# Kernel optimization log

Measured on AMD Instinct MI355X. Metric: run time of the kernel, lower is better.

Reference implementation:

```python
import jax, jax.numpy as jnp
import numpy as np

NUM_EMBEDDINGS = 1024
EMBEDDING_DIM = 256
BETA = 0.25


def setup_inputs() -> dict:
    key = jax.random.key(0)
    k1, k2 = jax.random.split(key)
    x = jax.random.normal(k1, (32, 256, 32, 32), dtype=jnp.float32)
    # nn.Embedding weight init: uniform(-1/K, 1/K)
    lim = 1.0 / NUM_EMBEDDINGS
    emb_weight = jax.random.uniform(k2, (NUM_EMBEDDINGS, EMBEDDING_DIM),
                                    dtype=jnp.float32, minval=-lim, maxval=lim)
    return {"x": x, "emb_weight": emb_weight}


def reference(x, emb_weight):
    b, c, h, w = x.shape
    # [b, h, w, c] -> [N, c]
    x_flat = jnp.transpose(x, (0, 2, 3, 1)).reshape(-1, c)
    distances = (jnp.sum(x_flat * x_flat, axis=1, keepdims=True)
                 - 2.0 * jnp.einsum('nc,kc->nk', x_flat, emb_weight)
                 + jnp.sum(emb_weight * emb_weight, axis=1))
    indices = jnp.argmin(distances, axis=1)  # [N]
    quantized = emb_weight[indices].reshape(b, h, w, c).transpose(0, 3, 1, 2)
    sg = jax.lax.stop_gradient
    commitment_loss = jnp.mean((sg(quantized) - x) ** 2)
    embedding_loss = jnp.mean((quantized - sg(x)) ** 2)
    loss = commitment_loss + BETA * embedding_loss
    return quantized, loss, indices.reshape(b, h, w)
```

## Files before the change

kernel.cpp:

```cpp
#include <hip/hip_runtime.h>

#define LOSS_OFF 8388608
#define IDX_OFF  8388609

#define WS_SEE   0
#define WS_SXX   4096
#define WS_KEY   135168
#define WS_CNT   397312
#define WS_LOSS  397320
#define WS_WL    397328
#define WS_EP    528448

#define FLT_BIG  3.402823466e+38f
#define MARGIN   1.0e-4f

typedef __attribute__((ext_vector_type(8))) short  short8v;
typedef __attribute__((ext_vector_type(4))) float  float4v;

#define GLD16(gp, lp) __builtin_amdgcn_global_load_lds( \
    (const __attribute__((address_space(1))) unsigned int*)(gp), \
    (__attribute__((address_space(3))) unsigned int*)(lp), 16, 0, 0)

__device__ __forceinline__ float np_sumsq256(const float* __restrict__ p, int stride) {
    float s[2];
#pragma unroll
    for (int half = 0; half < 2; half++) {
        const float* a = p + half * 128 * stride;
        float r[8];
#pragma unroll
        for (int l = 0; l < 8; l++) {
            float v = a[l * stride];
            float sq = v * v;
            asm volatile("" : "+v"(sq));
            r[l] = sq;
        }
#pragma unroll
        for (int i = 8; i < 128; i += 8) {
#pragma unroll
            for (int l = 0; l < 8; l++) {
                float v = a[(i + l) * stride];
                float sq = v * v;
                asm volatile("" : "+v"(sq));
                r[l] = r[l] + sq;
            }
        }
        s[half] = ((r[0] + r[1]) + (r[2] + r[3])) + ((r[4] + r[5]) + (r[6] + r[7]));
    }
    return s[0] + s[1];
}

__device__ __forceinline__ unsigned int f32_sortable(float m) {
    unsigned int u = __float_as_uint(m);
    return u ^ (((unsigned int)((int)u >> 31)) | 0x80000000u);
}
__device__ __forceinline__ float f32_unsortable(unsigned int s) {
    const unsigned int u = (s >> 31) ? (s ^ 0x80000000u) : ~s;
    return __uint_as_float(u);
}

__device__ __forceinline__ unsigned short f2bf(float f) {
    unsigned int u = __float_as_uint(f);
    return (unsigned short)((u + 0x7fffu + ((u >> 16) & 1u)) >> 16);
}
__device__ __forceinline__ float bf2f(unsigned short h) {
    return __uint_as_float(((unsigned int)h) << 16);
}

__global__ __launch_bounds__(256) void k_prep(const float* __restrict__ emb,
                                              unsigned short* __restrict__ ebP,
                                              float* __restrict__ see,
                                              int* __restrict__ cnt,
                                              double* __restrict__ loss) {
    const int t = threadIdx.x, bb = blockIdx.x;
    if (bb < 256) {
        const int idx = bb * 256 + t;
        const int l  = idx & 63;
        const int ph = (idx >> 6) & 1;
        const int ct = (idx >> 7) & 7;
        const int cc = (idx >> 10) & 7;
        const int cg = (idx >> 13) & 7;
        const int row = cg * 128 + ct * 16 + (l & 15);
        const int col = cc * 32 + (l >> 4) * 8;
        const float* src = emb + (size_t)row * 256 + col;
        uint4 out;
        unsigned short* op = (unsigned short*)&out;
#pragma unroll
        for (int i = 0; i < 8; i++) {
            const float v = src[i];
            const unsigned short h = f2bf(v);
            op[i] = ph ? f2bf(v - bf2f(h)) : h;
        }
        *(uint4*)(ebP + (size_t)idx * 8) = out;
    } else {
        const int k = (bb - 256) * 256 + t;
        see[k] = np_sumsq256(emb + (size_t)k * 256, 1);
        if (k == 0) { *cnt = 0; *loss = 0.0; }
    }
}

__global__ __launch_bounds__(256) void k_et(const float* __restrict__ emb,
                                            float* __restrict__ eT) {
    __shared__ float T[256][17];
    const int t  = threadIdx.x;
    const int k0 = blockIdx.x << 4;
    const int kr = t >> 4, cs = (t & 15) << 4;
#pragma unroll
    for (int j = 0; j < 4; j++) {
        const float4 v = *(const float4*)(emb + (size_t)(k0 + kr) * 256 + cs + j * 4);
        T[cs + j * 4 + 0][kr] = v.x;
        T[cs + j * 4 + 1][kr] = v.y;
        T[cs + j * 4 + 2][kr] = v.z;
        T[cs + j * 4 + 3][kr] = v.w;
    }
    __syncthreads();
    float* dst = eT + (size_t)t * 1024 + k0;
#pragma unroll
    for (int j = 0; j < 4; j++) {
        float4 v;
        v.x = T[t][j * 4 + 0]; v.y = T[t][j * 4 + 1];
        v.z = T[t][j * 4 + 2]; v.w = T[t][j * 4 + 3];
        *(float4*)(dst + j * 4) = v;
    }
}

__global__ __launch_bounds__(256) void k_xpack(const float* __restrict__ x,
                                               unsigned short* __restrict__ axP,
                                               float* __restrict__ sxx) {
    __shared__ float xs[256 * 33];
    const int t = threadIdx.x, rs = blockIdx.x;
    const int row = t & 31, cg = t >> 5;
    const int b = rs >> 5;
    const int hw0 = (rs & 31) << 5;
    const float* xb = x + (size_t)b * 262144 + hw0 + row;
#pragma unroll 4
    for (int cc2 = 0; cc2 < 32; cc2++) {
        const int c = cg * 32 + cc2;
        xs[c * 33 + row] = xb[(size_t)c * 1024];
    }
    __syncthreads();
#pragma unroll
    for (int ii = 0; ii < 4; ii++) {
        const int ci = ii * 256 + t;
        const int l = ci & 63;
        const int rowg = (ci >> 6) & 1;
        const int cc = ci >> 7;
        const int r = rowg * 16 + (l & 15);
        const int c0 = cc * 32 + (l >> 4) * 8;
        uint4 hp, lp;
        unsigned short* hpp = (unsigned short*)&hp;
        unsigned short* lpp = (unsigned short*)&lp;
#pragma unroll
        for (int i = 0; i < 8; i++) {
            const float v = xs[(c0 + i) * 33 + r];
            const unsigned short h = f2bf(v);
            hpp[i] = h;
            lpp[i] = f2bf(v - bf2f(h));
        }
        const size_t base = ((size_t)rs * 8 + cc) * 2 + rowg;
        *(uint4*)(axP + ((base * 2 + 0) * 64 + l) * 8) = hp;
        *(uint4*)(axP + ((base * 2 + 1) * 64 + l) * 8) = lp;
    }
    if (t < 32) sxx[rs * 32 + t] = np_sumsq256(xs + t, 33);
}

__global__ __launch_bounds__(512, 2) void k1_mfma(
        const unsigned short* __restrict__ axP,
        const unsigned short* __restrict__ ebP,
        const float* __restrict__ see_g,
        unsigned long long* __restrict__ key,
        int* __restrict__ cnt, int* __restrict__ wl) {
    __shared__ char smem[8192];
    unsigned long long* lk1 = (unsigned long long*)smem;
    float*              lg2 = (float*)(smem + 4096);
    const int t = threadIdx.x;
    const int codeg = t >> 6, l = t & 63;
    const int lrow = l >> 4, lcol = l & 15;
    const int rb = blockIdx.x;
    const int n0 = rb * 64;
    const char* aBase = (const char*)axP;
    char* aDst = smem + codeg * 1024;

    float4v acc[4][8];
#pragma unroll
    for (int at = 0; at < 4; at++)
#pragma unroll
        for (int ct = 0; ct < 8; ct++) acc[at][ct] = (float4v){0.f, 0.f, 0.f, 0.f};

    for (int cc = 0; cc < 8; cc++) {
        __syncthreads();
        {
            const int sub = codeg >> 2;
            const char* src = aBase + ((size_t)((rb * 2 + sub) * 8 + cc)) * 4096
                              + (size_t)(codeg & 3) * 1024 + (size_t)l * 16;
            GLD16(src, aDst);
        }
        __syncthreads();
        short8v ah[4], al[4];
#pragma unroll
        for (int at = 0; at < 4; at++) {
            const int off = (at >> 1) * 4096 + (at & 1) * 2048;
            ah[at] = *(const short8v*)(smem + off + l * 16);
            al[at] = *(const short8v*)(smem + off + 1024 + l * 16);
        }
#pragma unroll
        for (int ct = 0; ct < 8; ct++) {
            const size_t bb = ((((size_t)codeg * 8 + cc) * 8 + ct) * 2) * 512 + (size_t)l * 8;
            const short8v bh = *(const short8v*)(ebP + bb);
            const short8v bl = *(const short8v*)(ebP + bb + 512);
#pragma unroll
            for (int at = 0; at < 4; at++) {
                acc[at][ct] = __builtin_amdgcn_mfma_f32_16x16x32_bf16(ah[at], bh, acc[at][ct], 0, 0, 0);
                acc[at][ct] = __builtin_amdgcn_mfma_f32_16x16x32_bf16(ah[at], bl, acc[at][ct], 0, 0, 0);
                acc[at][ct] = __builtin_amdgcn_mfma_f32_16x16x32_bf16(al[at], bh, acc[at][ct], 0, 0, 0);
            }
        }
    }
    __syncthreads();

    float sv[8];
#pragma unroll
    for (int ct = 0; ct < 8; ct++) sv[ct] = see_g[codeg * 128 + ct * 16 + lcol];

#pragma unroll
    for (int at = 0; at < 4; at++) {
#pragma unroll
        for (int j = 0; j < 4; j++) {
            unsigned long long K1 = ~0ull; float G1 = FLT_BIG, G2 = FLT_BIG;
#pragma unroll
            for (int ct = 0; ct < 8; ct++) {
                const float g = fmaf(-2.f, acc[at][ct][j], sv[ct]);
                const int k = codeg * 128 + ct * 16 + lcol;
                const unsigned long long pk =
                    ((unsigned long long)f32_sortable(g) << 32) | (unsigned int)k;
                if (pk < K1) { G2 = G1; K1 = pk; G1 = g; }
                else         { G2 = fminf(G2, g); }
            }
#pragma unroll
            for (int m = 1; m < 16; m <<= 1) {
                const unsigned long long oK = __shfl_xor(K1, m, 64);
                const float oG2 = __shfl_xor(G2, m, 64);
                const float oG1 = f32_unsortable((unsigned int)(oK >> 32));
                if (oK < K1) { G2 = fminf(oG2, G1); K1 = oK; G1 = oG1; }
                else         { G2 = fminf(G2, oG1); }
            }
            const int rloc = at * 16 + lrow * 4 + j;
            if (lcol == 0) { lk1[rloc * 8 + codeg] = K1; lg2[rloc * 8 + codeg] = G2; }
        }
    }
    __syncthreads();
    if (t < 64) {
        unsigned long long K1 = ~0ull; float G1 = FLT_BIG, G2 = FLT_BIG;
        for (int cg = 0; cg < 8; cg++) {
            const unsigned long long oK = lk1[t * 8 + cg];
            const float oG2 = lg2[t * 8 + cg];
            const float oG1 = f32_unsortable((unsigned int)(oK >> 32));
            if (oK < K1) { G2 = fminf(oG2, G1); K1 = oK; G1 = oG1; }
            else         { G2 = fminf(G2, oG1); }
        }
        const int n = n0 + t;
        if (G2 - G1 > MARGIN) { key[n] = K1; }
        else { key[n] = ~0ull; wl[atomicAdd(cnt, 1)] = n; }
    }
}

__global__ __launch_bounds__(256) void k2r(const float* __restrict__ x,
                                           const float* __restrict__ eT,
                                           const float* __restrict__ see,
                                           const float* __restrict__ sxx,
                                           unsigned long long* __restrict__ key,
                                           const int* __restrict__ cnt,
                                           const int* __restrict__ wl) {
    __shared__ float xs[8][264];
    const int t = threadIdx.x;
    const int total = *cnt;
    for (int base = blockIdx.x * 8; base < total; base += 128 * 8) {
        int nrow[8]; float sx8[8];
#pragma unroll
        for (int r = 0; r < 8; r++) {
            int idx = base + r; if (idx >= total) idx = total - 1;
            const int n = wl[idx];
            nrow[r] = n; sx8[r] = sxx[n];
        }
        __syncthreads();
#pragma unroll
        for (int r = 0; r < 8; r++) {
            const int n = nrow[r];
            xs[r][t] = x[(size_t)(n >> 10) * 262144 + (size_t)t * 1024 + (n & 1023)];
        }
        __syncthreads();
        float d[8][4];
#pragma unroll
        for (int r = 0; r < 8; r++)
#pragma unroll
            for (int j = 0; j < 4; j++) d[r][j] = 0.f;
#pragma unroll 4
        for (int c = 0; c < 256; c++) {
            float ev[4];
#pragma unroll
            for (int j = 0; j < 4; j++) ev[j] = eT[(size_t)c * 1024 + t + 256 * j];
#pragma unroll
            for (int r = 0; r < 8; r++) {
                const float xv = xs[r][c];
                d[r][0] = fmaf(xv, ev[0], d[r][0]);
                d[r][1] = fmaf(xv, ev[1], d[r][1]);
                d[r][2] = fmaf(xv, ev[2], d[r][2]);
                d[r][3] = fmaf(xv, ev[3], d[r][3]);
            }
        }
#pragma unroll
        for (int r = 0; r < 8; r++) {
            unsigned long long best = ~0ull;
#pragma unroll
            for (int j = 0; j < 4; j++) {
                const float q = fmaf(-2.f, d[r][j], sx8[r]) + see[t + 256 * j];
                const unsigned long long pk =
                    ((unsigned long long)f32_sortable(q) << 32) | (unsigned int)(t + 256 * j);
                best = pk < best ? pk : best;
            }
            atomicMin(&key[nrow[r]], best);
        }
    }
}

__global__ __launch_bounds__(256) void k3_out(const float* __restrict__ x,
                                              const float* __restrict__ emb,
                                              const unsigned long long* __restrict__ key,
                                              float* __restrict__ dout,
                                              double* __restrict__ loss) {
    __shared__ float elds[32][257];
    __shared__ int   idxs[32];
    __shared__ float red[256];
    const int t  = threadIdx.x;
    const int bh = blockIdx.x;
    const int b = bh >> 5, h = bh & 31;
    if (t < 32) idxs[t] = (int)(key[(bh << 5) + t] & 0xffffffffull);
    __syncthreads();
    for (int r = 0; r < 32; r++) elds[r][t] = emb[(size_t)idxs[r] * 256 + t];
    __syncthreads();
    const int w = t & 31, cg = t >> 5;
    const size_t base = (size_t)b * 262144 + (size_t)(h * 32 + w);
    float acc = 0.f;
#pragma unroll 4
    for (int s = 0; s < 32; s++) {
        const int c = (cg << 5) + s;
        const float q  = elds[w][c];
        const float xv = x[base + (size_t)c * 1024];
        dout[base + (size_t)c * 1024] = q;
        const float d = q - xv;
        acc = fmaf(d, d, acc);
    }
    red[t] = acc;
    __syncthreads();
    for (int s = 128; s > 0; s >>= 1) {
        if (t < s) red[t] += red[t + s];
        __syncthreads();
    }
    if (t == 0) atomicAdd(loss, (double)red[0]);
    if (t < 32) dout[IDX_OFF + (bh << 5) + t] = (float)idxs[t];
}

__global__ void k4_fin(const double* __restrict__ loss, float* __restrict__ dout) {
    dout[LOSS_OFF] = (float)(1.25 * (*loss) / 8388608.0);
}

extern "C" void kernel_launch(void* const* d_in, const int* in_sizes, int n_in,
                              void* d_out, int out_size, void* d_ws, size_t ws_size,
                              hipStream_t stream) {
    const float* x   = (const float*)d_in[0];
    const float* emb = (const float*)d_in[1];
    float* dout = (float*)d_out;
    char* ws = (char*)d_ws;
    float*  see  = (float*)(ws + WS_SEE);
    float*  sxx  = (float*)(ws + WS_SXX);
    unsigned long long* key = (unsigned long long*)(ws + WS_KEY);
    int*    cnt  = (int*)(ws + WS_CNT);
    double* loss = (double*)(ws + WS_LOSS);
    int*    wl   = (int*)(ws + WS_WL);
    unsigned short* ebP = (unsigned short*)(ws + WS_EP);
    float*  eT   = (float*)(ws + WS_EP);
    unsigned short* axP = (unsigned short*)d_out;

    k_prep <<<260,  256, 0, stream>>>(emb, ebP, see, cnt, loss);
    k_xpack<<<1024, 256, 0, stream>>>(x, axP, sxx);
    k1_mfma<<<512,  512, 0, stream>>>(axP, ebP, see, key, cnt, wl);
    k_et   <<<64,   256, 0, stream>>>(emb, eT);
    k2r    <<<128,  256, 0, stream>>>(x, eT, see, sxx, key, cnt, wl);
    k3_out <<<1024, 256, 0, stream>>>(x, emb, key, dout, loss);
    k4_fin <<<1,      1, 0, stream>>>(loss, dout);
}
```

Baseline: 204.6 us.

## Derive loss from min distances, preload all A chunks into LDS, raise MFMA priority

The loss is now computed as the sum of ||x||^2 plus the winning distance term kept from the MFMA argmin, in a small new reduction kernel. This lets the output kernel skip re-reading x, which removes a full pass over the input. The MFMA kernel now stages all eight A chunks into about 70KB of LDS with a single barrier instead of syncing per chunk, and wraps the MFMA bursts in s_setprio. The risks are lower occupancy from the larger LDS footprint and a slight loss-precision change: ambiguous rows keep the bf16-split approximate distance rather than the refined one.

```diff
diff --git a/kernel.cpp b/kernel.cpp
--- a/kernel.cpp
+++ b/kernel.cpp
@@ -168,37 +168,41 @@
         const unsigned short* __restrict__ ebP,
         const float* __restrict__ see_g,
         unsigned long long* __restrict__ key,
+        float* __restrict__ distg,
         int* __restrict__ cnt, int* __restrict__ wl) {
-    __shared__ char smem[8192];
-    unsigned long long* lk1 = (unsigned long long*)smem;
-    float*              lg2 = (float*)(smem + 4096);
+    __shared__ char smem[71680];
+    unsigned long long* lk1 = (unsigned long long*)(smem + 65536);
+    float*              lg2 = (float*)(smem + 69632);
     const int t = threadIdx.x;
     const int codeg = t >> 6, l = t & 63;
     const int lrow = l >> 4, lcol = l & 15;
     const int rb = blockIdx.x;
     const int n0 = rb * 64;
-    const char* aBase = (const char*)axP;
-    char* aDst = smem + codeg * 1024;
-
-    float4v acc[4][8];
-#pragma unroll
-    for (int at = 0; at < 4; at++)
-#pragma unroll
-        for (int ct = 0; ct < 8; ct++) acc[at][ct] = (float4v){0.f, 0.f, 0.f, 0.f};
-
-    for (int cc = 0; cc < 8; cc++) {
-        __syncthreads();
-        {
-            const int sub = codeg >> 2;
+
+    {
+        const int sub = codeg >> 2;
+        const char* aBase = (const char*)axP;
+        char* aDst = smem + codeg * 1024;
+#pragma unroll
+        for (int cc = 0; cc < 8; cc++) {
             const char* src = aBase + ((size_t)((rb * 2 + sub) * 8 + cc)) * 4096
                               + (size_t)(codeg & 3) * 1024 + (size_t)l * 16;
-            GLD16(src, aDst);
-        }
-        __syncthreads();
+            GLD16(src, aDst + cc * 8192);
+        }
+    }
+    __syncthreads();
+
+    float4v acc[4][8];
+#pragma unroll
+    for (int at = 0; at < 4; at++)
+#pragma unroll
+        for (int ct = 0; ct < 8; ct++) acc[at][ct] = (float4v){0.f, 0.f, 0.f, 0.f};
+
+    for (int cc = 0; cc < 8; cc++) {
         short8v ah[4], al[4];
 #pragma unroll
         for (int at = 0; at < 4; at++) {
-            const int off = (at >> 1) * 4096 + (at & 1) * 2048;
+            const int off = cc * 8192 + (at >> 1) * 4096 + (at & 1) * 2048;
             ah[at] = *(const short8v*)(smem + off + l * 16);
             al[at] = *(const short8v*)(smem + off + 1024 + l * 16);
         }
@@ -207,15 +211,16 @@
             const size_t bb = ((((size_t)codeg * 8 + cc) * 8 + ct) * 2) * 512 + (size_t)l * 8;
             const short8v bh = *(const short8v*)(ebP + bb);
             const short8v bl = *(const short8v*)(ebP + bb + 512);
+            __builtin_amdgcn_s_setprio(1);
 #pragma unroll
             for (int at = 0; at < 4; at++) {
                 acc[at][ct] = __builtin_amdgcn_mfma_f32_16x16x32_bf16(ah[at], bh, acc[at][ct], 0, 0, 0);
                 acc[at][ct] = __builtin_amdgcn_mfma_f32_16x16x32_bf16(ah[at], bl, acc[at][ct], 0, 0, 0);
                 acc[at][ct] = __builtin_amdgcn_mfma_f32_16x16x32_bf16(al[at], bh, acc[at][ct], 0, 0, 0);
             }
-        }
-    }
-    __syncthreads();
+            __builtin_amdgcn_s_setprio(0);
+        }
+    }
 
     float sv[8];
 #pragma unroll
@@ -258,6 +263,7 @@
             else         { G2 = fminf(G2, oG1); }
         }
         const int n = n0 + t;
+        distg[n] = G1;
         if (G2 - G1 > MARGIN) { key[n] = K1; }
         else { key[n] = ~0ull; wl[atomicAdd(cnt, 1)] = n; }
     }
@@ -322,14 +328,32 @@
     }
 }
 
-__global__ __launch_bounds__(256) void k3_out(const float* __restrict__ x,
-                                              const float* __restrict__ emb,
+__global__ __launch_bounds__(256) void k_loss(const float* __restrict__ sxx,
+                                              const float* __restrict__ distg,
+                                              double* __restrict__ loss) {
+    __shared__ double red[256];
+    const int t = threadIdx.x;
+    const int base = blockIdx.x * 1024 + t;
+    double sd = 0.0;
+#pragma unroll
+    for (int i = 0; i < 4; i++) {
+        const int n = base + i * 256;
+        sd += (double)(sxx[n] + distg[n]);
+    }
+    red[t] = sd;
+    __syncthreads();
+    for (int s = 128; s > 0; s >>= 1) {
+        if (t < s) red[t] += red[t + s];
+        __syncthreads();
+    }
+    if (t == 0) atomicAdd(loss, red[0]);
+}
+
+__global__ __launch_bounds__(256) void k3_out(const float* __restrict__ emb,
                                               const unsigned long long* __restrict__ key,
-                                              float* __restrict__ dout,
-                                              double* __restrict__ loss) {
+                                              float* __restrict__ dout) {
     __shared__ float elds[32][257];
     __shared__ int   idxs[32];
-    __shared__ float red[256];
     const int t  = threadIdx.x;
     const int bh = blockIdx.x;
     const int b = bh >> 5, h = bh & 31;
@@ -339,23 +363,11 @@
     __syncthreads();
     const int w = t & 31, cg = t >> 5;
     const size_t base = (size_t)b * 262144 + (size_t)(h * 32 + w);
-    float acc = 0.f;
 #pragma unroll 4
     for (int s = 0; s < 32; s++) {
         const int c = (cg << 5) + s;
-        const float q  = elds[w][c];
-        const float xv = x[base + (size_t)c * 1024];
-        dout[base + (size_t)c * 1024] = q;
-        const float d = q - xv;
-        acc = fmaf(d, d, acc);
-    }
-    red[t] = acc;
-    __syncthreads();
-    for (int s = 128; s > 0; s >>= 1) {
-        if (t < s) red[t] += red[t + s];
-        __syncthreads();
-    }
-    if (t == 0) atomicAdd(loss, (double)red[0]);
+        dout[base + (size_t)c * 1024] = elds[w][c];
+    }
     if (t < 32) dout[IDX_OFF + (bh << 5) + t] = (float)idxs[t];
 }
 
@@ -379,12 +391,14 @@
     unsigned short* ebP = (unsigned short*)(ws + WS_EP);
     float*  eT   = (float*)(ws + WS_EP);
     unsigned short* axP = (unsigned short*)d_out;
+    float* distg = dout + IDX_OFF;
 
     k_prep <<<260,  256, 0, stream>>>(emb, ebP, see, cnt, loss);
     k_xpack<<<1024, 256, 0, stream>>>(x, axP, sxx);
-    k1_mfma<<<512,  512, 0, stream>>>(axP, ebP, see, key, cnt, wl);
+    k1_mfma<<<512,  512, 0, stream>>>(axP, ebP, see, key, distg, cnt, wl);
     k_et   <<<64,   256, 0, stream>>>(emb, eT);
     k2r    <<<128,  256, 0, stream>>>(x, eT, see, sxx, key, cnt, wl);
-    k3_out <<<1024, 256, 0, stream>>>(x, emb, key, dout, loss);
+    k_loss <<<32,   256, 0, stream>>>(sxx, distg, loss);
+    k3_out <<<1024, 256, 0, stream>>>(emb, key, dout);
     k4_fin <<<1,      1, 0, stream>>>(loss, dout);
 }
```

After: 200.0 us. 1.02x faster.
